# Optimization experiments

Measured on AMD Instinct MI355X. Metric: run time of the kernel, lower is better.

Reference implementation:

```python
import jax, jax.numpy as jnp
import numpy as np

NUM_HEADS = 8
HIDDEN_DIM = 256
QUERY_DIM = 256
HEAD_DIM = HIDDEN_DIM // NUM_HEADS
NORM_FACT = float(HIDDEN_DIM / NUM_HEADS) ** (-0.5)


def setup_inputs() -> dict:
    key = jax.random.key(0)
    k1, k2, k3, k4, k5 = jax.random.split(key, 5)
    B, Q, H, W = 16, 100, 64, 64
    q = jax.random.normal(k1, (B, Q, QUERY_DIM), dtype=jnp.float32)
    k = jax.random.normal(k2, (B, QUERY_DIM, H, W), dtype=jnp.float32)
    mask = jax.random.randint(k3, (B, H, W), 0, 2).astype(jnp.bool_)
    # xavier_uniform for [hidden, query] linear weights
    limit = float(np.sqrt(6.0 / (HIDDEN_DIM + QUERY_DIM)))
    Wq = jax.random.uniform(k4, (HIDDEN_DIM, QUERY_DIM), minval=-limit, maxval=limit, dtype=jnp.float32)
    Wk = jax.random.uniform(k5, (HIDDEN_DIM, QUERY_DIM), minval=-limit, maxval=limit, dtype=jnp.float32)
    bq = jnp.zeros((HIDDEN_DIM,), dtype=jnp.float32)
    bk = jnp.zeros((HIDDEN_DIM,), dtype=jnp.float32)
    return {"q": q, "k": k, "Wq": Wq, "bq": bq, "Wk": Wk, "bk": bk, "mask": mask}


def reference(q, k, Wq, bq, Wk, bk, mask):
    B, Q, _ = q.shape
    _, C, H, W = k.shape
    # q projection: [B, Q, hidden]
    qp = jnp.einsum('bqc,hc->bqh', q, Wq) + bq
    # k projection via 1x1 conv == channelwise linear: [B, hidden, H, W]
    kp = jnp.einsum('bchw,oc->bohw', k, Wk) + bk[None, :, None, None]
    # split heads: qh [B,Q,nh,hd], kh [B,nh,hd,H,W]
    qh = qp.reshape(B, Q, NUM_HEADS, HEAD_DIM)
    kh = kp.reshape(B, NUM_HEADS, HEAD_DIM, H, W)
    # scores [B,Q,nh,H,W]
    weights = jnp.einsum('bqnd,bndhw->bqnhw', qh, kh) * NORM_FACT
    # masked fill: mask [B,H,W] -> broadcast over (Q, heads)
    weights = jnp.where(mask[:, None, None, :, :], -jnp.inf, weights)
    # softmax jointly over (heads, H, W), as in torch flatten(2)
    flat = weights.reshape(B, Q, NUM_HEADS * H * W)
    flat = jax.nn.softmax(flat, axis=-1)
    return flat.reshape(B, Q, NUM_HEADS, H, W)
```

## Files before the change

### kernel.cpp

```cpp
#include <hip/hip_runtime.h>
#include <hip/hip_bf16.h>
#include <math.h>

#define BB 16
#define QQ 100
#define NH 8
#define HD 32
#define HWN 4096
#define NORM_FACT 0.17677669529663687f
#define QPAD 128
#define NSLOT 64

typedef short bf16x8_t __attribute__((ext_vector_type(8)));
typedef float f32x4_t  __attribute__((ext_vector_type(4)));

__device__ __forceinline__ unsigned short bf16bits(float f) {
    __hip_bfloat16 h = __float2bfloat16(f);
    return __builtin_bit_cast(unsigned short, h);
}
__device__ __forceinline__ float bf16tof(unsigned short u) {
    union { unsigned int i; float f; } x; x.i = (unsigned int)u << 16; return x.f;
}

__global__ void k_prep(const float* __restrict__ Wq, const float* __restrict__ Wk,
                       float* __restrict__ WqT, unsigned short* __restrict__ Wkbf) {
    int idx = blockIdx.x;
    int h = threadIdx.x;
    if (idx < 256) {
        WqT[idx * 256 + h] = Wq[h * 256 + idx];
    } else {
        int r = idx - 256;
        Wkbf[r * 256 + h] = bf16bits(Wk[r * 256 + h]);
    }
}

__global__ __launch_bounds__(256) void k_qproj(const float* __restrict__ q,
                                               const float* __restrict__ WqT,
                                               const float* __restrict__ bq,
                                               unsigned short* __restrict__ qphi,
                                               unsigned short* __restrict__ qplo) {
    int blk = blockIdx.x;
    int b = blk >> 5, q0 = (blk & 31) * 4;
    int h = threadIdx.x;
    size_t obase = ((size_t)b * QPAD + q0) * 256 + h;
    if (q0 >= QQ) {
#pragma unroll
        for (int i = 0; i < 4; ++i) { qphi[obase + i * 256] = 0; qplo[obase + i * 256] = 0; }
        return;
    }
    __shared__ float qsh[4][256];
    int ibase = (b * QQ + q0) * 256;
#pragma unroll
    for (int i = 0; i < 4; ++i) qsh[i][h] = q[ibase + i * 256 + h];
    __syncthreads();
    float bias = bq[h];
    float a0 = bias, a1 = bias, a2 = bias, a3 = bias;
    for (int c = 0; c < 256; ++c) {
        float wv = WqT[c * 256 + h];
        a0 = fmaf(qsh[0][c], wv, a0);
        a1 = fmaf(qsh[1][c], wv, a1);
        a2 = fmaf(qsh[2][c], wv, a2);
        a3 = fmaf(qsh[3][c], wv, a3);
    }
    float a[4] = {a0 * NORM_FACT, a1 * NORM_FACT, a2 * NORM_FACT, a3 * NORM_FACT};
#pragma unroll
    for (int i = 0; i < 4; ++i) {
        unsigned short hi = bf16bits(a[i]);
        qphi[obase + i * 256] = hi;
        qplo[obase + i * 256] = bf16bits(a[i] - bf16tof(hi));
    }
}

__global__ __launch_bounds__(256) void k_tconv(const float* __restrict__ k,
                                               unsigned short* __restrict__ kT) {
    int b = blockIdx.z, c0 = blockIdx.y * 64, hw0 = blockIdx.x * 64;
    int t = threadIdx.x;
    __shared__ float lds[64][65];
    const float* src = k + ((size_t)b * 256 + c0) * HWN + hw0;
    int col = t & 63, r0 = t >> 6;
#pragma unroll
    for (int i = 0; i < 16; ++i) {
        int r = i * 4 + r0;
        lds[r][col] = src[(size_t)r * HWN + col];
    }
    __syncthreads();
    int hw = t >> 2, cc = (t & 3) * 16;
    unsigned short* dst = kT + ((size_t)b * HWN + hw0 + hw) * 256 + c0 + cc;
    uint4 v0, v1;
    unsigned int* w0 = (unsigned int*)&v0;
    unsigned int* w1 = (unsigned int*)&v1;
#pragma unroll
    for (int j = 0; j < 4; ++j) {
        w0[j] = (unsigned int)bf16bits(lds[cc + 2*j + 0][hw])
              | ((unsigned int)bf16bits(lds[cc + 2*j + 1][hw]) << 16);
        w1[j] = (unsigned int)bf16bits(lds[cc + 8 + 2*j + 0][hw])
              | ((unsigned int)bf16bits(lds[cc + 8 + 2*j + 1][hw]) << 16);
    }
    *(uint4*)(dst)     = v0;
    *(uint4*)(dst + 8) = v1;
}

__global__ __launch_bounds__(256) void k_kproj(const unsigned short* __restrict__ kT,
                                               const unsigned short* __restrict__ Wkbf,
                                               const float* __restrict__ bk,
                                               unsigned short* __restrict__ kpT) {
    int b = blockIdx.y;
    int hwblk = blockIdx.x * 64;
    int t = threadIdx.x;
    int w = t >> 6, lane = t & 63;
    int n15 = lane & 15;
    int kg = lane >> 4;
    int hw = hwblk + w * 16 + n15;

    f32x4_t acc[16];
#pragma unroll
    for (int m = 0; m < 16; ++m) acc[m] = f32x4_t{0.f, 0.f, 0.f, 0.f};

    const unsigned short* kTrow = kT + ((size_t)b * HWN + hw) * 256 + kg * 8;
    const unsigned short* wbase = Wkbf + (size_t)n15 * 256 + kg * 8;

#pragma unroll 2
    for (int ks = 0; ks < 8; ++ks) {
        bf16x8_t bfrag = *reinterpret_cast<const bf16x8_t*>(kTrow + ks * 32);
#pragma unroll
        for (int m = 0; m < 16; ++m) {
            bf16x8_t afrag = *reinterpret_cast<const bf16x8_t*>(wbase + (size_t)m * 16 * 256 + ks * 32);
            acc[m] = __builtin_amdgcn_mfma_f32_16x16x32_bf16(afrag, bfrag, acc[m], 0, 0, 0);
        }
    }

    __shared__ unsigned short tile2[64 * 264];
    int hw_l = w * 16 + n15;
#pragma unroll
    for (int m = 0; m < 16; ++m) {
        ushort4 pk;
        unsigned short* pkp = (unsigned short*)&pk;
#pragma unroll
        for (int r = 0; r < 4; ++r) {
            int o = m * 16 + kg * 4 + r;
            pkp[r] = bf16bits(acc[m][r] + bk[o]);
        }
        *(ushort4*)&tile2[hw_l * 264 + m * 16 + kg * 4] = pk;
    }
    __syncthreads();
    int hw_r = t >> 2, sub = t & 3;
    unsigned short* dst = kpT + ((size_t)b * HWN + hwblk + hw_r) * 256;
#pragma unroll
    for (int j = 0; j < 8; ++j) {
        int o = j * 32 + sub * 8;
        uint4 v = *(uint4*)&tile2[hw_r * 264 + o];
        *(uint4*)(dst + o) = v;
    }
}

__global__ __launch_bounds__(256) void k_sums(const unsigned short* __restrict__ qphi,
                                              const unsigned short* __restrict__ qplo,
                                              const unsigned short* __restrict__ kpT,
                                              const int* __restrict__ mask,
                                              float* __restrict__ partial) {
    int hws = blockIdx.x, qt = blockIdx.y, b = blockIdx.z;
    int t = threadIdx.x, w = t >> 6, lane = t & 63;
    int n15 = lane & 15, kg = lane >> 4;
    int hw0 = hws * 256 + w * 64;
    float mm[4];
#pragma unroll
    for (int ht = 0; ht < 4; ++ht)
        mm[ht] = mask[b * HWN + hw0 + ht * 16 + n15] ? 0.0f : 1.0f;
    const unsigned short* ahi_b = qphi + ((size_t)(b * QPAD + qt * 32 + n15)) * 256 + kg * 8;
    const unsigned short* alo_b = qplo + ((size_t)(b * QPAD + qt * 32 + n15)) * 256 + kg * 8;
    const unsigned short* brow  = kpT  + ((size_t)(b * HWN + hw0 + n15)) * 256 + kg * 8;
    float sums[2][4] = {};
#pragma unroll 1
    for (int n = 0; n < NH; ++n) {
        bf16x8_t bf[4];
#pragma unroll
        for (int ht = 0; ht < 4; ++ht)
            bf[ht] = *reinterpret_cast<const bf16x8_t*>(brow + (size_t)(ht * 16) * 256 + n * 32);
#pragma unroll
        for (int mt = 0; mt < 2; ++mt) {
            bf16x8_t ahi = *reinterpret_cast<const bf16x8_t*>(ahi_b + (size_t)(mt * 16) * 256 + n * 32);
            bf16x8_t alo = *reinterpret_cast<const bf16x8_t*>(alo_b + (size_t)(mt * 16) * 256 + n * 32);
#pragma unroll
            for (int ht = 0; ht < 4; ++ht) {
                f32x4_t acc = {0.f, 0.f, 0.f, 0.f};
                acc = __builtin_amdgcn_mfma_f32_16x16x32_bf16(ahi, bf[ht], acc, 0, 0, 0);
                acc = __builtin_amdgcn_mfma_f32_16x16x32_bf16(alo, bf[ht], acc, 0, 0, 0);
#pragma unroll
                for (int r = 0; r < 4; ++r)
                    sums[mt][r] += __expf(acc[r]) * mm[ht];
            }
        }
    }
#pragma unroll
    for (int mt = 0; mt < 2; ++mt)
#pragma unroll
        for (int r = 0; r < 4; ++r) {
            float v = sums[mt][r];
            v += __shfl_xor(v, 1, 64);
            v += __shfl_xor(v, 2, 64);
            v += __shfl_xor(v, 4, 64);
            v += __shfl_xor(v, 8, 64);
            if (n15 == 0) {
                int qrow = qt * 32 + mt * 16 + kg * 4 + r;
                partial[((size_t)b * QPAD + qrow) * NSLOT + hws * 4 + w] = v;
            }
        }
}

__global__ void k_invsum(const float* __restrict__ partial, float* __restrict__ inv) {
    int i = blockIdx.x * 256 + threadIdx.x;
    if (i < BB * QQ) {
        int b = i / QQ, qq = i % QQ;
        const float* p = partial + ((size_t)b * QPAD + qq) * NSLOT;
        float s = 0.0f;
#pragma unroll
        for (int j = 0; j < NSLOT; ++j) s += p[j];
        inv[i] = 1.0f / s;
    }
}

__global__ __launch_bounds__(256) void k_write(const unsigned short* __restrict__ qphi,
                                               const unsigned short* __restrict__ qplo,
                                               const unsigned short* __restrict__ kpT,
                                               const int* __restrict__ mask,
                                               const float* __restrict__ inv,
                                               float* __restrict__ out) {
    int hws = blockIdx.x, qt = blockIdx.y, b = blockIdx.z;
    int t = threadIdx.x, w = t >> 6, lane = t & 63;
    int n15 = lane & 15, kg = lane >> 4;
    int hw0 = hws * 256 + w * 64;
    float mm[4];
#pragma unroll
    for (int ht = 0; ht < 4; ++ht)
        mm[ht] = mask[b * HWN + hw0 + ht * 16 + n15] ? 0.0f : 1.0f;
    float invq[2][4];
#pragma unroll
    for (int mt = 0; mt < 2; ++mt)
#pragma unroll
        for (int r = 0; r < 4; ++r) {
            int qrow = qt * 32 + mt * 16 + kg * 4 + r;
            invq[mt][r] = (qrow < QQ) ? inv[b * QQ + qrow] : 0.0f;
        }
    const unsigned short* ahi_b = qphi + ((size_t)(b * QPAD + qt * 32 + n15)) * 256 + kg * 8;
    const unsigned short* alo_b = qplo + ((size_t)(b * QPAD + qt * 32 + n15)) * 256 + kg * 8;
    const unsigned short* brow  = kpT  + ((size_t)(b * HWN + hw0 + n15)) * 256 + kg * 8;
    __shared__ float lt[4][16][65];
#pragma unroll 1
    for (int n = 0; n < NH; ++n) {
        bf16x8_t bf[4];
#pragma unroll
        for (int ht = 0; ht < 4; ++ht)
            bf[ht] = *reinterpret_cast<const bf16x8_t*>(brow + (size_t)(ht * 16) * 256 + n * 32);
#pragma unroll 1
        for (int mt = 0; mt < 2; ++mt) {
            bf16x8_t ahi = *reinterpret_cast<const bf16x8_t*>(ahi_b + (size_t)(mt * 16) * 256 + n * 32);
            bf16x8_t alo = *reinterpret_cast<const bf16x8_t*>(alo_b + (size_t)(mt * 16) * 256 + n * 32);
#pragma unroll
            for (int ht = 0; ht < 4; ++ht) {
                f32x4_t acc = {0.f, 0.f, 0.f, 0.f};
                acc = __builtin_amdgcn_mfma_f32_16x16x32_bf16(ahi, bf[ht], acc, 0, 0, 0);
                acc = __builtin_amdgcn_mfma_f32_16x16x32_bf16(alo, bf[ht], acc, 0, 0, 0);
#pragma unroll
                for (int r = 0; r < 4; ++r)
                    lt[w][kg * 4 + r][ht * 16 + n15] = __expf(acc[r]) * mm[ht] * invq[mt][r];
            }
            __syncthreads();
#pragma unroll
            for (int rr = 0; rr < 16; ++rr) {
                int qrow = qt * 32 + mt * 16 + rr;
                if (qrow < QQ)
                    out[(((size_t)(b * QQ + qrow)) * NH + n) * HWN + hw0 + lane] = lt[w][rr][lane];
            }
            __syncthreads();
        }
    }
}

extern "C" void kernel_launch(void* const* d_in, const int* in_sizes, int n_in,
                              void* d_out, int out_size, void* d_ws, size_t ws_size,
                              hipStream_t stream) {
    const float* q    = (const float*)d_in[0];
    const float* k    = (const float*)d_in[1];
    const float* Wq   = (const float*)d_in[2];
    const float* bq   = (const float*)d_in[3];
    const float* Wk   = (const float*)d_in[4];
    const float* bk   = (const float*)d_in[5];
    const int*   mask = (const int*)d_in[6];
    float* out = (float*)d_out;

    char* base = (char*)d_ws;
    unsigned short* kT   = (unsigned short*)(base);
    unsigned short* kpT  = (unsigned short*)(base + 33554432);
    unsigned short* qphi = (unsigned short*)(base + 67108864);
    unsigned short* qplo = (unsigned short*)(base + 68157440);
    float*  WqT     = (float*)(base + 69206016);
    unsigned short* Wkbf = (unsigned short*)(base + 69468160);
    float*  partial = (float*)(base + 69599232);
    float*  inv     = (float*)(base + 70123520);
    if (ws_size < (size_t)70129920) return;

    k_prep  <<<dim3(512), dim3(256), 0, stream>>>(Wq, Wk, WqT, Wkbf);
    k_qproj <<<dim3(512), dim3(256), 0, stream>>>(q, WqT, bq, qphi, qplo);
    k_tconv <<<dim3(64, 4, 16), dim3(256), 0, stream>>>(k, kT);
    k_kproj <<<dim3(64, 16), dim3(256), 0, stream>>>(kT, Wkbf, bk, kpT);
    k_sums  <<<dim3(16, 4, 16), dim3(256), 0, stream>>>(qphi, qplo, kpT, mask, partial);
    k_invsum<<<dim3(7), dim3(256), 0, stream>>>(partial, inv);
    k_write <<<dim3(16, 4, 16), dim3(256), 0, stream>>>(qphi, qplo, kpT, mask, inv, out);
}
```

Baseline: 216.6 us.

## Fuse softmax-denominator pass into k projection and shrink query padding

Folds the exp-sum pass into the k-projection kernel, reusing the projected keys already held in LDS instead of reading them back from global memory. Query padding drops from 128 to 112 rows, so the write kernel uses 16-row query tiles across 7 tiles and does less work on padded rows. The inverse-sum kernel becomes a block-per-row reduction over 256 partial slots. In exchange, each fused block now iterates over all 7 query tiles with 28 accumulators, which raises register pressure, and the kernel count falls by one launch.

Result: slower. 233.1 us (+7.6%).

```diff
diff --git a/kernel.cpp b/kernel.cpp
--- a/kernel.cpp
+++ b/kernel.cpp
@@ -8,8 +8,7 @@
 #define HD 32
 #define HWN 4096
 #define NORM_FACT 0.17677669529663687f
-#define QPAD 128
-#define NSLOT 64
+#define QPAD 112
 
 typedef short bf16x8_t __attribute__((ext_vector_type(8)));
 typedef float f32x4_t  __attribute__((ext_vector_type(4)));
@@ -40,7 +39,7 @@
                                                unsigned short* __restrict__ qphi,
                                                unsigned short* __restrict__ qplo) {
     int blk = blockIdx.x;
-    int b = blk >> 5, q0 = (blk & 31) * 4;
+    int b = blk / 28, q0 = (blk % 28) * 4;
     int h = threadIdx.x;
     size_t obase = ((size_t)b * QPAD + q0) * 256 + h;
     if (q0 >= QQ) {
@@ -100,10 +99,14 @@
     *(uint4*)(dst + 8) = v1;
 }
 
-__global__ __launch_bounds__(256) void k_kproj(const unsigned short* __restrict__ kT,
+__global__ __launch_bounds__(256) void k_fused(const unsigned short* __restrict__ kT,
                                                const unsigned short* __restrict__ Wkbf,
                                                const float* __restrict__ bk,
-                                               unsigned short* __restrict__ kpT) {
+                                               const unsigned short* __restrict__ qphi,
+                                               const unsigned short* __restrict__ qplo,
+                                               const int* __restrict__ mask,
+                                               unsigned short* __restrict__ kpT,
+                                               float* __restrict__ partial) {
     int b = blockIdx.y;
     int hwblk = blockIdx.x * 64;
     int t = threadIdx.x;
@@ -143,6 +146,7 @@
         *(ushort4*)&tile2[hw_l * 264 + m * 16 + kg * 4] = pk;
     }
     __syncthreads();
+
     int hw_r = t >> 2, sub = t & 3;
     unsigned short* dst = kpT + ((size_t)b * HWN + hwblk + hw_r) * 256;
 #pragma unroll
@@ -151,48 +155,28 @@
         uint4 v = *(uint4*)&tile2[hw_r * 264 + o];
         *(uint4*)(dst + o) = v;
     }
-}
-
-__global__ __launch_bounds__(256) void k_sums(const unsigned short* __restrict__ qphi,
-                                              const unsigned short* __restrict__ qplo,
-                                              const unsigned short* __restrict__ kpT,
-                                              const int* __restrict__ mask,
-                                              float* __restrict__ partial) {
-    int hws = blockIdx.x, qt = blockIdx.y, b = blockIdx.z;
-    int t = threadIdx.x, w = t >> 6, lane = t & 63;
-    int n15 = lane & 15, kg = lane >> 4;
-    int hw0 = hws * 256 + w * 64;
-    float mm[4];
-#pragma unroll
-    for (int ht = 0; ht < 4; ++ht)
-        mm[ht] = mask[b * HWN + hw0 + ht * 16 + n15] ? 0.0f : 1.0f;
-    const unsigned short* ahi_b = qphi + ((size_t)(b * QPAD + qt * 32 + n15)) * 256 + kg * 8;
-    const unsigned short* alo_b = qplo + ((size_t)(b * QPAD + qt * 32 + n15)) * 256 + kg * 8;
-    const unsigned short* brow  = kpT  + ((size_t)(b * HWN + hw0 + n15)) * 256 + kg * 8;
-    float sums[2][4] = {};
+
+    float mm = mask[b * HWN + hw] ? 0.0f : 1.0f;
+    const unsigned short* ahi_b = qphi + ((size_t)(b * QPAD + n15)) * 256 + kg * 8;
+    const unsigned short* alo_b = qplo + ((size_t)(b * QPAD + n15)) * 256 + kg * 8;
+    float sums[7][4] = {};
 #pragma unroll 1
     for (int n = 0; n < NH; ++n) {
-        bf16x8_t bf[4];
-#pragma unroll
-        for (int ht = 0; ht < 4; ++ht)
-            bf[ht] = *reinterpret_cast<const bf16x8_t*>(brow + (size_t)(ht * 16) * 256 + n * 32);
-#pragma unroll
-        for (int mt = 0; mt < 2; ++mt) {
+        bf16x8_t bfr = *reinterpret_cast<const bf16x8_t*>(&tile2[hw_l * 264 + n * 32 + kg * 8]);
+#pragma unroll
+        for (int mt = 0; mt < 7; ++mt) {
             bf16x8_t ahi = *reinterpret_cast<const bf16x8_t*>(ahi_b + (size_t)(mt * 16) * 256 + n * 32);
             bf16x8_t alo = *reinterpret_cast<const bf16x8_t*>(alo_b + (size_t)(mt * 16) * 256 + n * 32);
-#pragma unroll
-            for (int ht = 0; ht < 4; ++ht) {
-                f32x4_t acc = {0.f, 0.f, 0.f, 0.f};
-                acc = __builtin_amdgcn_mfma_f32_16x16x32_bf16(ahi, bf[ht], acc, 0, 0, 0);
-                acc = __builtin_amdgcn_mfma_f32_16x16x32_bf16(alo, bf[ht], acc, 0, 0, 0);
-#pragma unroll
-                for (int r = 0; r < 4; ++r)
-                    sums[mt][r] += __expf(acc[r]) * mm[ht];
-            }
-        }
-    }
-#pragma unroll
-    for (int mt = 0; mt < 2; ++mt)
+            f32x4_t a2 = {0.f, 0.f, 0.f, 0.f};
+            a2 = __builtin_amdgcn_mfma_f32_16x16x32_bf16(ahi, bfr, a2, 0, 0, 0);
+            a2 = __builtin_amdgcn_mfma_f32_16x16x32_bf16(alo, bfr, a2, 0, 0, 0);
+#pragma unroll
+            for (int r = 0; r < 4; ++r)
+                sums[mt][r] += __expf(a2[r]) * mm;
+        }
+    }
+#pragma unroll
+    for (int mt = 0; mt < 7; ++mt)
 #pragma unroll
         for (int r = 0; r < 4; ++r) {
             float v = sums[mt][r];
@@ -201,22 +185,25 @@
             v += __shfl_xor(v, 4, 64);
             v += __shfl_xor(v, 8, 64);
             if (n15 == 0) {
-                int qrow = qt * 32 + mt * 16 + kg * 4 + r;
-                partial[((size_t)b * QPAD + qrow) * NSLOT + hws * 4 + w] = v;
+                int qrow = mt * 16 + kg * 4 + r;
+                partial[((size_t)b * QPAD + qrow) * 256 + blockIdx.x * 4 + w] = v;
             }
         }
 }
 
-__global__ void k_invsum(const float* __restrict__ partial, float* __restrict__ inv) {
-    int i = blockIdx.x * 256 + threadIdx.x;
-    if (i < BB * QQ) {
-        int b = i / QQ, qq = i % QQ;
-        const float* p = partial + ((size_t)b * QPAD + qq) * NSLOT;
-        float s = 0.0f;
-#pragma unroll
-        for (int j = 0; j < NSLOT; ++j) s += p[j];
-        inv[i] = 1.0f / s;
-    }
+__global__ __launch_bounds__(256) void k_invsum(const float* __restrict__ partial,
+                                                float* __restrict__ inv) {
+    int blk = blockIdx.x;
+    int b = blk / QQ, qq = blk % QQ;
+    const float* p = partial + ((size_t)b * QPAD + qq) * 256;
+    int t = threadIdx.x;
+    float v = p[t];
+#pragma unroll
+    for (int off = 32; off; off >>= 1) v += __shfl_xor(v, off, 64);
+    __shared__ float red[4];
+    if ((t & 63) == 0) red[t >> 6] = v;
+    __syncthreads();
+    if (t == 0) inv[blk] = 1.0f / (red[0] + red[1] + red[2] + red[3]);
 }
 
 __global__ __launch_bounds__(256) void k_write(const unsigned short* __restrict__ qphi,
@@ -233,16 +220,14 @@
 #pragma unroll
     for (int ht = 0; ht < 4; ++ht)
         mm[ht] = mask[b * HWN + hw0 + ht * 16 + n15] ? 0.0f : 1.0f;
-    float invq[2][4];
-#pragma unroll
-    for (int mt = 0; mt < 2; ++mt)
-#pragma unroll
-        for (int r = 0; r < 4; ++r) {
-            int qrow = qt * 32 + mt * 16 + kg * 4 + r;
-            invq[mt][r] = (qrow < QQ) ? inv[b * QQ + qrow] : 0.0f;
-        }
-    const unsigned short* ahi_b = qphi + ((size_t)(b * QPAD + qt * 32 + n15)) * 256 + kg * 8;
-    const unsigned short* alo_b = qplo + ((size_t)(b * QPAD + qt * 32 + n15)) * 256 + kg * 8;
+    float invq[4];
+#pragma unroll
+    for (int r = 0; r < 4; ++r) {
+        int qrow = qt * 16 + kg * 4 + r;
+        invq[r] = (qrow < QQ) ? inv[b * QQ + qrow] : 0.0f;
+    }
+    const unsigned short* ahi_b = qphi + ((size_t)(b * QPAD + qt * 16 + n15)) * 256 + kg * 8;
+    const unsigned short* alo_b = qplo + ((size_t)(b * QPAD + qt * 16 + n15)) * 256 + kg * 8;
     const unsigned short* brow  = kpT  + ((size_t)(b * HWN + hw0 + n15)) * 256 + kg * 8;
     __shared__ float lt[4][16][65];
 #pragma unroll 1
@@ -251,28 +236,25 @@
 #pragma unroll
         for (int ht = 0; ht < 4; ++ht)
             bf[ht] = *reinterpret_cast<const bf16x8_t*>(brow + (size_t)(ht * 16) * 256 + n * 32);
-#pragma unroll 1
-        for (int mt = 0; mt < 2; ++mt) {
-            bf16x8_t ahi = *reinterpret_cast<const bf16x8_t*>(ahi_b + (size_t)(mt * 16) * 256 + n * 32);
-            bf16x8_t alo = *reinterpret_cast<const bf16x8_t*>(alo_b + (size_t)(mt * 16) * 256 + n * 32);
-#pragma unroll
-            for (int ht = 0; ht < 4; ++ht) {
-                f32x4_t acc = {0.f, 0.f, 0.f, 0.f};
-                acc = __builtin_amdgcn_mfma_f32_16x16x32_bf16(ahi, bf[ht], acc, 0, 0, 0);
-                acc = __builtin_amdgcn_mfma_f32_16x16x32_bf16(alo, bf[ht], acc, 0, 0, 0);
-#pragma unroll
-                for (int r = 0; r < 4; ++r)
-                    lt[w][kg * 4 + r][ht * 16 + n15] = __expf(acc[r]) * mm[ht] * invq[mt][r];
-            }
-            __syncthreads();
-#pragma unroll
-            for (int rr = 0; rr < 16; ++rr) {
-                int qrow = qt * 32 + mt * 16 + rr;
-                if (qrow < QQ)
-                    out[(((size_t)(b * QQ + qrow)) * NH + n) * HWN + hw0 + lane] = lt[w][rr][lane];
-            }
-            __syncthreads();
-        }
+        bf16x8_t ahi = *reinterpret_cast<const bf16x8_t*>(ahi_b + n * 32);
+        bf16x8_t alo = *reinterpret_cast<const bf16x8_t*>(alo_b + n * 32);
+#pragma unroll
+        for (int ht = 0; ht < 4; ++ht) {
+            f32x4_t acc = {0.f, 0.f, 0.f, 0.f};
+            acc = __builtin_amdgcn_mfma_f32_16x16x32_bf16(ahi, bf[ht], acc, 0, 0, 0);
+            acc = __builtin_amdgcn_mfma_f32_16x16x32_bf16(alo, bf[ht], acc, 0, 0, 0);
+#pragma unroll
+            for (int r = 0; r < 4; ++r)
+                lt[w][kg * 4 + r][ht * 16 + n15] = __expf(acc[r]) * mm[ht] * invq[r];
+        }
+        __syncthreads();
+#pragma unroll
+        for (int rr = 0; rr < 16; ++rr) {
+            int qrow = qt * 16 + rr;
+            if (qrow < QQ)
+                out[(((size_t)(b * QQ + qrow)) * NH + n) * HWN + hw0 + lane] = lt[w][rr][lane];
+        }
+        __syncthreads();
     }
 }
 
@@ -292,18 +274,17 @@
     unsigned short* kT   = (unsigned short*)(base);
     unsigned short* kpT  = (unsigned short*)(base + 33554432);
     unsigned short* qphi = (unsigned short*)(base + 67108864);
-    unsigned short* qplo = (unsigned short*)(base + 68157440);
-    float*  WqT     = (float*)(base + 69206016);
-    unsigned short* Wkbf = (unsigned short*)(base + 69468160);
-    float*  partial = (float*)(base + 69599232);
-    float*  inv     = (float*)(base + 70123520);
-    if (ws_size < (size_t)70129920) return;
+    unsigned short* qplo = (unsigned short*)(base + 68026368);
+    float*  WqT     = (float*)(base + 68943872);
+    unsigned short* Wkbf = (unsigned short*)(base + 69206016);
+    float*  partial = (float*)(base + 69337088);
+    float*  inv     = (float*)(base + 71172096);
+    if (ws_size < (size_t)71178496) return;
 
     k_prep  <<<dim3(512), dim3(256), 0, stream>>>(Wq, Wk, WqT, Wkbf);
-    k_qproj <<<dim3(512), dim3(256), 0, stream>>>(q, WqT, bq, qphi, qplo);
+    k_qproj <<<dim3(448), dim3(256), 0, stream>>>(q, WqT, bq, qphi, qplo);
     k_tconv <<<dim3(64, 4, 16), dim3(256), 0, stream>>>(k, kT);
-    k_kproj <<<dim3(64, 16), dim3(256), 0, stream>>>(kT, Wkbf, bk, kpT);
-    k_sums  <<<dim3(16, 4, 16), dim3(256), 0, stream>>>(qphi, qplo, kpT, mask, partial);
-    k_invsum<<<dim3(7), dim3(256), 0, stream>>>(partial, inv);
-    k_write <<<dim3(16, 4, 16), dim3(256), 0, stream>>>(qphi, qplo, kpT, mask, inv, out);
-}
+    k_fused <<<dim3(64, 16), dim3(256), 0, stream>>>(kT, Wkbf, bk, qphi, qplo, mask, kpT, partial);
+    k_invsum<<<dim3(1600), dim3(256), 0, stream>>>(partial, inv);
+    k_write <<<dim3(16, 7, 16), dim3(256), 0, stream>>>(qphi, qplo, kpT, mask, inv, out);
+}
```
